# Optimization experiments

Measured on AMD Instinct MI355X. Metric: run time of the kernel, lower is better.

The kernel has to match this reference:

```python
import jax, jax.numpy as jnp
import numpy as np

N_NODES = 50000
HEADS = 4
OUT_DIM = 64
NEG_SLOPE = 0.2
BETA = 0.5
C_CONST = 1.0
EPS = 1e-16


def setup_inputs() -> dict:
    key = jax.random.key(0)
    ks = jax.random.split(key, 6)
    in_dim = 128
    x = jax.random.normal(ks[0], (N_NODES, in_dim), dtype=jnp.float32)
    edge_index = jax.random.randint(ks[1], (2, 800000), 0, N_NODES, dtype=jnp.int64)
    # GATConv params (glorot-ish scale)
    W = jax.random.normal(ks[2], (in_dim, HEADS * OUT_DIM), dtype=jnp.float32) * (1.0 / np.sqrt(in_dim))
    att_src = jax.random.normal(ks[3], (HEADS, OUT_DIM), dtype=jnp.float32) * (1.0 / np.sqrt(OUT_DIM))
    att_dst = jax.random.normal(ks[4], (HEADS, OUT_DIM), dtype=jnp.float32) * (1.0 / np.sqrt(OUT_DIM))
    bias = jnp.zeros((HEADS * OUT_DIM,), dtype=jnp.float32)
    return {"x": x, "edge_index": edge_index, "W": W, "att_src": att_src,
            "att_dst": att_dst, "bias": bias}


def _gat_conv(x, edge_index, W, att_src, att_dst, bias):
    N = x.shape[0]
    # add self loops (PyG GATConv default)
    loop = jnp.arange(N, dtype=edge_index.dtype)
    src = jnp.concatenate([edge_index[0], loop])
    dst = jnp.concatenate([edge_index[1], loop])
    # linear transform: [N, H, F]
    h = (x @ W).reshape(N, HEADS, OUT_DIM)
    # per-node attention logits: [N, H]
    a_src = jnp.einsum('nhf,hf->nh', h, att_src)
    a_dst = jnp.einsum('nhf,hf->nh', h, att_dst)
    # per-edge logits and segment softmax over destination nodes
    e = jax.nn.leaky_relu(a_src[src] + a_dst[dst], negative_slope=NEG_SLOPE)  # [E, H]
    m = jax.ops.segment_max(e, dst, num_segments=N)                           # [N, H]
    ex = jnp.exp(e - m[dst])
    s = jax.ops.segment_sum(ex, dst, num_segments=N)                          # [N, H]
    alpha = ex / (s[dst] + EPS)                                               # [E, H]
    # aggregate messages: [N, H, F]
    out = jax.ops.segment_sum(alpha[:, :, None] * h[src], dst, num_segments=N)
    return out.reshape(N, HEADS * OUT_DIM) + bias


def reference(x, edge_index, W, att_src, att_dst, bias):
    # eval mode: feature dropout and attention dropout are identity
    z = _gat_conv(x, edge_index, W, att_src, att_dst, bias)
    return BETA * z + (C_CONST - BETA) * jax.nn.elu(z)
```

## Files before the change

kernel.cpp:

```cpp
#include <hip/hip_runtime.h>
#include <hip/hip_bf16.h>

typedef unsigned short u16;
typedef __attribute__((ext_vector_type(8))) short bf16x8;
typedef __attribute__((ext_vector_type(4))) float f32x4;

#define HEADS 4
#define OUT_DIM 64
#define HF 256
#define IN_DIM 128
#define NEG_SLOPE 0.2f
#define EPSF 1e-16f

__device__ __forceinline__ float braw2f(u16 u) {
    union { float f; unsigned int i; } c; c.i = ((unsigned int)u) << 16; return c.f;
}
__device__ __forceinline__ u16 f2braw(float v) {
    __hip_bfloat16 t = __float2bfloat16(v);
    return *(u16*)&t;
}
__device__ __forceinline__ float lrelu(float e) { return e < 0.f ? NEG_SLOPE * e : e; }

__device__ __forceinline__ bool detect_i64(const int* ei) {
    return (ei[1] | ei[3] | ei[5] | ei[7] | ei[9] | ei[11] | ei[13] | ei[15]) == 0;
}
__device__ __forceinline__ void get_edge(const int* ei, int E, int t, bool i64,
                                         int& s, int& d) {
    if (t < E) {
        if (i64) { s = ei[2 * t]; d = ei[2 * (E + t)]; }
        else     { s = ei[t];     d = ei[E + t]; }
    } else {
        s = d = t - E;
    }
}

__global__ __launch_bounds__(256) void init_kernel(const float* __restrict__ W,
                                                   const float* __restrict__ att_s,
                                                   const float* __restrict__ att_d,
                                                   float* __restrict__ wa_s,
                                                   float* __restrict__ wa_d,
                                                   int* __restrict__ cnt,
                                                   int* __restrict__ cur,
                                                   int* __restrict__ gcnt,
                                                   int N, int NZ) {
    int b = blockIdx.x;
    if (b == 0 && threadIdx.x == 0) *gcnt = 0;
    if (b < NZ) {
        int i = b * 256 + threadIdx.x;
        if (i < N) { cnt[i] = 0; cur[i] = 0; }
    } else {
        for (int idx = threadIdx.x; idx < HEADS * IN_DIM; idx += 256) {
            int h = idx >> 7, k = idx & 127;
            float ss = 0.f, sd = 0.f;
            for (int f = 0; f < OUT_DIM; ++f) {
                float wv = W[k * HF + h * OUT_DIM + f];
                ss = fmaf(wv, att_s[h * OUT_DIM + f], ss);
                sd = fmaf(wv, att_d[h * OUT_DIM + f], sd);
            }
            wa_s[idx] = ss;
            wa_d[idx] = sd;
        }
    }
}

__global__ __launch_bounds__(256) void phase1_kernel(const float* __restrict__ x,
                                                     const int* __restrict__ ei,
                                                     const float* __restrict__ W,
                                                     const float* __restrict__ wa_s,
                                                     const float* __restrict__ wa_d,
                                                     float* __restrict__ a_src,
                                                     float* __restrict__ a_dst,
                                                     u16* __restrict__ xb,
                                                     u16* __restrict__ Wfrag,
                                                     int* __restrict__ cnt,
                                                     int N, int E, int NA, int NC) {
    int b = blockIdx.x;
    if (b < NA) {
        int wid = threadIdx.x >> 6;
        int l = threadIdx.x & 63;
        int g = l >> 4, c = l & 15, kc = c * 8;
        int v = b * 16 + wid * 4 + g;
        if (v >= N) return;

        const float4* xr = (const float4*)(x + (size_t)v * IN_DIM + kc);
        float4 x0 = xr[0], x1 = xr[1];

        uint4 u;
        u.x = (unsigned)f2braw(x0.x) | ((unsigned)f2braw(x0.y) << 16);
        u.y = (unsigned)f2braw(x0.z) | ((unsigned)f2braw(x0.w) << 16);
        u.z = (unsigned)f2braw(x1.x) | ((unsigned)f2braw(x1.y) << 16);
        u.w = (unsigned)f2braw(x1.z) | ((unsigned)f2braw(x1.w) << 16);
        *(uint4*)(xb + (size_t)v * IN_DIM + kc) = u;

        float ps[4], pd[4];
        #pragma unroll
        for (int h = 0; h < 4; ++h) {
            const float4* s4 = (const float4*)(wa_s + h * IN_DIM + kc);
            const float4* d4 = (const float4*)(wa_d + h * IN_DIM + kc);
            float4 s0 = s4[0], s1 = s4[1], d0 = d4[0], d1 = d4[1];
            ps[h] = x0.x*s0.x + x0.y*s0.y + x0.z*s0.z + x0.w*s0.w
                  + x1.x*s1.x + x1.y*s1.y + x1.z*s1.z + x1.w*s1.w;
            pd[h] = x0.x*d0.x + x0.y*d0.y + x0.z*d0.z + x0.w*d0.w
                  + x1.x*d1.x + x1.y*d1.y + x1.z*d1.z + x1.w*d1.w;
        }
        #pragma unroll
        for (int off = 1; off < 16; off <<= 1) {
            #pragma unroll
            for (int h = 0; h < 4; ++h) {
                ps[h] += __shfl_xor(ps[h], off);
                pd[h] += __shfl_xor(pd[h], off);
            }
        }
        if (c == 0) {
            float4 vs, vd;
            vs.x = ps[0]; vs.y = ps[1]; vs.z = ps[2]; vs.w = ps[3];
            vd.x = pd[0]; vd.y = pd[1]; vd.z = pd[2]; vd.w = pd[3];
            *(float4*)(a_src + (size_t)v * HEADS) = vs;
            *(float4*)(a_dst + (size_t)v * HEADS) = vd;
        }
    } else if (b < NA + NC) {
        int t = (b - NA) * 256 + threadIdx.x;
        if (t >= E + N) return;
        bool i64 = detect_i64(ei);
        int src, dst; get_edge(ei, E, t, i64, src, dst);
        if (src >= 0 && src < N && dst >= 0 && dst < N) atomicAdd(cnt + dst, 1);
    } else {
        int bb = b - NA - NC;
        for (int idx = bb * 256 + threadIdx.x; idx < 32768; idx += 8 * 256) {
            int j = idx & 7, l = (idx >> 3) & 63, t = (idx >> 9) & 3;
            int s = (idx >> 11) & 3, h = (idx >> 13) & 3;
            int k = s * 32 + ((l >> 4) & 3) * 8 + j;
            int col = h * OUT_DIM + t * 16 + (l & 15);
            Wfrag[idx] = f2braw(W[k * HF + col]);
        }
    }
}

__global__ __launch_bounds__(256) void offset_kernel(const int* __restrict__ cnt,
                                                     int* __restrict__ offs,
                                                     int* __restrict__ gcnt, int N) {
    int idx = blockIdx.x * 256 + threadIdx.x;
    int l = threadIdx.x & 63;
    int d = (idx < N) ? cnt[idx] : 0;
    int s = d;
    #pragma unroll
    for (int off = 1; off < 64; off <<= 1) {
        int t = __shfl_up(s, off);
        if (l >= off) s += t;
    }
    int base = 0;
    if (l == 63) base = atomicAdd(gcnt, s);
    base = __shfl(base, 63);
    if (idx < N) offs[idx] = base + s - d;
}

__global__ __launch_bounds__(256) void fill_kernel(const int* __restrict__ ei,
                                                   const int* __restrict__ offs,
                                                   int* __restrict__ cur,
                                                   int* __restrict__ slots,
                                                   uint2* __restrict__ wslots,
                                                   const float* __restrict__ a_src,
                                                   const float* __restrict__ a_dst,
                                                   int E, int N) {
    int t = blockIdx.x * 256 + threadIdx.x;
    if (t >= E + N) return;
    bool i64 = detect_i64(ei);
    int src, dst; get_edge(ei, E, t, i64, src, dst);
    if (src >= 0 && src < N && dst >= 0 && dst < N) {
        int pos = atomicAdd(cur + dst, 1);
        int idx = offs[dst] + pos;
        slots[idx] = src;
        if (wslots) {
            float4 as = ((const float4*)a_src)[src];
            float4 ad = ((const float4*)a_dst)[dst];
            float w0 = __expf(lrelu(as.x + ad.x));
            float w1 = __expf(lrelu(as.y + ad.y));
            float w2 = __expf(lrelu(as.z + ad.z));
            float w3 = __expf(lrelu(as.w + ad.w));
            uint2 wp;
            wp.x = (unsigned)f2braw(w0) | ((unsigned)f2braw(w1) << 16);
            wp.y = (unsigned)f2braw(w2) | ((unsigned)f2braw(w3) << 16);
            wslots[idx] = wp;
        }
    }
}

#define ACC_EDGE(wp, r) do { \
    float w0_ = braw2f((wp).x & 0xffff), w1_ = braw2f((wp).x >> 16); \
    float w2_ = braw2f((wp).y & 0xffff), w3_ = braw2f((wp).y >> 16); \
    ls0 += w0_; ls1 += w1_; ls2 += w2_; ls3 += w3_; \
    float xv_[8]; \
    xv_[0] = braw2f((r).x & 0xffff); xv_[1] = braw2f((r).x >> 16); \
    xv_[2] = braw2f((r).y & 0xffff); xv_[3] = braw2f((r).y >> 16); \
    xv_[4] = braw2f((r).z & 0xffff); xv_[5] = braw2f((r).z >> 16); \
    xv_[6] = braw2f((r).w & 0xffff); xv_[7] = braw2f((r).w >> 16); \
    _Pragma("unroll") \
    for (int q_ = 0; q_ < 8; ++q_) { \
        G0[q_] = fmaf(w0_, xv_[q_], G0[q_]); \
        G1[q_] = fmaf(w1_, xv_[q_], G1[q_]); \
        G2[q_] = fmaf(w2_, xv_[q_], G2[q_]); \
        G3[q_] = fmaf(w3_, xv_[q_], G3[q_]); \
    } \
} while (0)

__global__ __launch_bounds__(512) void fused_gz_kernel(const int* __restrict__ offs,
                                                       const int* __restrict__ cnt,
                                                       const int* __restrict__ slots,
                                                       const uint2* __restrict__ wslots,
                                                       const u16* __restrict__ xb,
                                                       const u16* __restrict__ Wfrag,
                                                       const float* __restrict__ bias,
                                                       float* __restrict__ out,
                                                       int N, int ET) {
    __shared__ u16 smem[32 * 520];

    int tid = threadIdx.x;
    int wid = tid >> 6;
    int l = tid & 63;
    int g = l >> 4, c = l & 15, kc = c * 8;
    int n = wid * 4 + g;
    int v = blockIdx.x * 32 + n;

    int beg = 0, end = 0;
    if (v < N) {
        beg = offs[v];
        int deg = cnt[v];
        beg = max(0, min(beg, ET));
        end = max(beg, min(beg + deg, ET));
    }

    float ls0 = 0.f, ls1 = 0.f, ls2 = 0.f, ls3 = 0.f;
    float G0[8] = {0,0,0,0,0,0,0,0};
    float G1[8] = {0,0,0,0,0,0,0,0};
    float G2[8] = {0,0,0,0,0,0,0,0};
    float G3[8] = {0,0,0,0,0,0,0,0};

    int j = beg;
    for (; j + 4 <= end; j += 4) {
        int s0 = max(0, min(slots[j],     N - 1));
        int s1 = max(0, min(slots[j + 1], N - 1));
        int s2 = max(0, min(slots[j + 2], N - 1));
        int s3 = max(0, min(slots[j + 3], N - 1));
        uint2 wp0 = wslots[j];
        uint2 wp1 = wslots[j + 1];
        uint2 wp2 = wslots[j + 2];
        uint2 wp3 = wslots[j + 3];
        uint4 r0 = *(const uint4*)(xb + (size_t)s0 * IN_DIM + kc);
        uint4 r1 = *(const uint4*)(xb + (size_t)s1 * IN_DIM + kc);
        uint4 r2 = *(const uint4*)(xb + (size_t)s2 * IN_DIM + kc);
        uint4 r3 = *(const uint4*)(xb + (size_t)s3 * IN_DIM + kc);
        ACC_EDGE(wp0, r0);
        ACC_EDGE(wp1, r1);
        ACC_EDGE(wp2, r2);
        ACC_EDGE(wp3, r3);
    }
    for (; j < end; ++j) {
        int s0 = max(0, min(slots[j], N - 1));
        uint2 wp0 = wslots[j];
        uint4 r0 = *(const uint4*)(xb + (size_t)s0 * IN_DIM + kc);
        ACC_EDGE(wp0, r0);
    }

    if (v < N) {
        float i0 = 1.f / (ls0 + EPSF), i1 = 1.f / (ls1 + EPSF);
        float i2 = 1.f / (ls2 + EPSF), i3 = 1.f / (ls3 + EPSF);
        u16* lp = smem + n * 520 + c * 8;
        #pragma unroll
        for (int h = 0; h < 4; ++h) {
            const float* G = h == 0 ? G0 : h == 1 ? G1 : h == 2 ? G2 : G3;
            float inv = h == 0 ? i0 : h == 1 ? i1 : h == 2 ? i2 : i3;
            uint4 u;
            u.x = (unsigned)f2braw(G[0] * inv) | ((unsigned)f2braw(G[1] * inv) << 16);
            u.y = (unsigned)f2braw(G[2] * inv) | ((unsigned)f2braw(G[3] * inv) << 16);
            u.z = (unsigned)f2braw(G[4] * inv) | ((unsigned)f2braw(G[5] * inv) << 16);
            u.w = (unsigned)f2braw(G[6] * inv) | ((unsigned)f2braw(G[7] * inv) << 16);
            *(uint4*)(lp + h * 128) = u;
        }
    }
    __syncthreads();

    int t = wid >> 2;
    int h = wid & 3;
    int q = l >> 4, mcol = l & 15;
    int nb = blockIdx.x * 32 + t * 16;

    const u16* lp = smem + (t * 16 + mcol) * 520 + h * 128 + q * 8;
    bf16x8 A[4];
    A[0] = *(const bf16x8*)(lp);
    A[1] = *(const bf16x8*)(lp + 32);
    A[2] = *(const bf16x8*)(lp + 64);
    A[3] = *(const bf16x8*)(lp + 96);

    f32x4 acc0 = {0.f,0.f,0.f,0.f}, acc1 = acc0, acc2 = acc0, acc3 = acc0;
    #pragma unroll
    for (int s = 0; s < 4; ++s) {
        const u16* wb = Wfrag + (((h * 4 + s) * 4) << 9) + l * 8;
        bf16x8 B0 = *(const bf16x8*)(wb);
        bf16x8 B1 = *(const bf16x8*)(wb + 512);
        bf16x8 B2 = *(const bf16x8*)(wb + 1024);
        bf16x8 B3 = *(const bf16x8*)(wb + 1536);
        acc0 = __builtin_amdgcn_mfma_f32_16x16x32_bf16(A[s], B0, acc0, 0, 0, 0);
        acc1 = __builtin_amdgcn_mfma_f32_16x16x32_bf16(A[s], B1, acc1, 0, 0, 0);
        acc2 = __builtin_amdgcn_mfma_f32_16x16x32_bf16(A[s], B2, acc2, 0, 0, 0);
        acc3 = __builtin_amdgcn_mfma_f32_16x16x32_bf16(A[s], B3, acc3, 0, 0, 0);
    }

    #pragma unroll
    for (int bt = 0; bt < 4; ++bt) {
        f32x4 a = bt == 0 ? acc0 : bt == 1 ? acc1 : bt == 2 ? acc2 : acc3;
        float b = bias[h * OUT_DIM + bt * 16 + mcol];
        #pragma unroll
        for (int r = 0; r < 4; ++r) {
            int vv = nb + q * 4 + r;
            if (vv < N) {
                float z = a[r] + b;
                float y = z > 0.f ? z : 0.5f * z + 0.5f * (__expf(z) - 1.f);
                out[(size_t)vv * HF + h * OUT_DIM + bt * 16 + mcol] = y;
            }
        }
    }
}

__global__ __launch_bounds__(512) void gather_bf_kernel(const int* __restrict__ offs,
                                                        const int* __restrict__ cnt,
                                                        const int* __restrict__ slots,
                                                        const u16* __restrict__ xb,
                                                        const float* __restrict__ a_src,
                                                        const float* __restrict__ a_dst,
                                                        u16* __restrict__ Gout, int N, int ET) {
    int v = (blockIdx.x * 512 + threadIdx.x) >> 6;
    int l = threadIdx.x & 63;
    if (v >= N) return;
    int h = l >> 4, c = l & 15, kc = c * 8;

    int beg = offs[v];
    int deg = cnt[v];
    beg = max(0, min(beg, ET));
    int end = max(beg, min(beg + deg, ET));
    float adh = a_dst[v * HEADS + h];

    float ls = 0.f;
    float G[8] = {0.f,0.f,0.f,0.f,0.f,0.f,0.f,0.f};

    int j = beg;
    for (; j + 4 <= end; j += 4) {
        int s0 = max(0, min(slots[j],     N - 1));
        int s1 = max(0, min(slots[j + 1], N - 1));
        int s2 = max(0, min(slots[j + 2], N - 1));
        int s3 = max(0, min(slots[j + 3], N - 1));
        float w0 = __expf(lrelu(a_src[s0 * HEADS + h] + adh));
        float w1 = __expf(lrelu(a_src[s1 * HEADS + h] + adh));
        float w2 = __expf(lrelu(a_src[s2 * HEADS + h] + adh));
        float w3 = __expf(lrelu(a_src[s3 * HEADS + h] + adh));
        uint4 r0 = *(const uint4*)(xb + (size_t)s0 * IN_DIM + kc);
        uint4 r1 = *(const uint4*)(xb + (size_t)s1 * IN_DIM + kc);
        uint4 r2 = *(const uint4*)(xb + (size_t)s2 * IN_DIM + kc);
        uint4 r3 = *(const uint4*)(xb + (size_t)s3 * IN_DIM + kc);
        ls += (w0 + w1) + (w2 + w3);
        unsigned ua[4];
        ua[0]=r0.x; ua[1]=r0.y; ua[2]=r0.z; ua[3]=r0.w;
        #pragma unroll
        for (int q = 0; q < 4; ++q) {
            G[2*q]   = fmaf(w0, braw2f(ua[q] & 0xffff), G[2*q]);
            G[2*q+1] = fmaf(w0, braw2f(ua[q] >> 16),    G[2*q+1]);
        }
        ua[0]=r1.x; ua[1]=r1.y; ua[2]=r1.z; ua[3]=r1.w;
        #pragma unroll
        for (int q = 0; q < 4; ++q) {
            G[2*q]   = fmaf(w1, braw2f(ua[q] & 0xffff), G[2*q]);
            G[2*q+1] = fmaf(w1, braw2f(ua[q] >> 16),    G[2*q+1]);
        }
        ua[0]=r2.x; ua[1]=r2.y; ua[2]=r2.z; ua[3]=r2.w;
        #pragma unroll
        for (int q = 0; q < 4; ++q) {
            G[2*q]   = fmaf(w2, braw2f(ua[q] & 0xffff), G[2*q]);
            G[2*q+1] = fmaf(w2, braw2f(ua[q] >> 16),    G[2*q+1]);
        }
        ua[0]=r3.x; ua[1]=r3.y; ua[2]=r3.z; ua[3]=r3.w;
        #pragma unroll
        for (int q = 0; q < 4; ++q) {
            G[2*q]   = fmaf(w3, braw2f(ua[q] & 0xffff), G[2*q]);
            G[2*q+1] = fmaf(w3, braw2f(ua[q] >> 16),    G[2*q+1]);
        }
    }
    for (; j < end; ++j) {
        int s0 = max(0, min(slots[j], N - 1));
        float w0 = __expf(lrelu(a_src[s0 * HEADS + h] + adh));
        uint4 r0 = *(const uint4*)(xb + (size_t)s0 * IN_DIM + kc);
        ls += w0;
        unsigned ua[4]; ua[0]=r0.x; ua[1]=r0.y; ua[2]=r0.z; ua[3]=r0.w;
        #pragma unroll
        for (int q = 0; q < 4; ++q) {
            G[2*q]   = fmaf(w0, braw2f(ua[q] & 0xffff), G[2*q]);
            G[2*q+1] = fmaf(w0, braw2f(ua[q] >> 16),    G[2*q+1]);
        }
    }

    float inv = 1.f / (ls + EPSF);
    uint4 u;
    u.x = (unsigned)f2braw(G[0] * inv) | ((unsigned)f2braw(G[1] * inv) << 16);
    u.y = (unsigned)f2braw(G[2] * inv) | ((unsigned)f2braw(G[3] * inv) << 16);
    u.z = (unsigned)f2braw(G[4] * inv) | ((unsigned)f2braw(G[5] * inv) << 16);
    u.w = (unsigned)f2braw(G[6] * inv) | ((unsigned)f2braw(G[7] * inv) << 16);
    *(uint4*)(Gout + (size_t)v * 512 + h * 128 + kc) = u;
}

__global__ __launch_bounds__(512) void gather_f32_kernel(const int* __restrict__ offs,
                                                         const int* __restrict__ cnt,
                                                         const int* __restrict__ slots,
                                                         const float* __restrict__ x,
                                                         const float* __restrict__ a_src,
                                                         const float* __restrict__ a_dst,
                                                         u16* __restrict__ Gout, int N, int ET) {
    int v = (blockIdx.x * 512 + threadIdx.x) >> 6;
    int l = threadIdx.x & 63;
    if (v >= N) return;
    int h = l >> 4, c = l & 15, kc = c * 8;

    int beg = offs[v];
    int deg = cnt[v];
    beg = max(0, min(beg, ET));
    int end = max(beg, min(beg + deg, ET));
    float adh = a_dst[v * HEADS + h];

    float ls = 0.f;
    float G[8] = {0.f,0.f,0.f,0.f,0.f,0.f,0.f,0.f};
    for (int j = beg; j < end; ++j) {
        int s0 = max(0, min(slots[j], N - 1));
        float w0 = __expf(lrelu(a_src[s0 * HEADS + h] + adh));
        const float4* xr0 = (const float4*)(x + (size_t)s0 * IN_DIM + kc);
        float4 a0 = xr0[0], b0 = xr0[1];
        ls += w0;
        G[0]=fmaf(w0,a0.x,G[0]); G[1]=fmaf(w0,a0.y,G[1]);
        G[2]=fmaf(w0,a0.z,G[2]); G[3]=fmaf(w0,a0.w,G[3]);
        G[4]=fmaf(w0,b0.x,G[4]); G[5]=fmaf(w0,b0.y,G[5]);
        G[6]=fmaf(w0,b0.z,G[6]); G[7]=fmaf(w0,b0.w,G[7]);
    }
    float inv = 1.f / (ls + EPSF);
    uint4 u;
    u.x = (unsigned)f2braw(G[0] * inv) | ((unsigned)f2braw(G[1] * inv) << 16);
    u.y = (unsigned)f2braw(G[2] * inv) | ((unsigned)f2braw(G[3] * inv) << 16);
    u.z = (unsigned)f2braw(G[4] * inv) | ((unsigned)f2braw(G[5] * inv) << 16);
    u.w = (unsigned)f2braw(G[6] * inv) | ((unsigned)f2braw(G[7] * inv) << 16);
    *(uint4*)(Gout + (size_t)v * 512 + h * 128 + kc) = u;
}

__global__ __launch_bounds__(256) void zgemm_kernel(const u16* __restrict__ Wfrag,
                                                    const float* __restrict__ bias,
                                                    float* __restrict__ out, int N) {
    int h = threadIdx.x >> 6;
    int l = threadIdx.x & 63;
    int q = l >> 4, mcol = l & 15;
    int nb = blockIdx.x * 16;

    const u16* G = (const u16*)out;
    bool valid = (nb + mcol) < N;
    int vA = valid ? nb + mcol : N - 1;
    const u16* gp = G + (size_t)vA * 512 + h * 128 + q * 8;
    bf16x8 A[4];
    A[0] = *(const bf16x8*)(gp);
    A[1] = *(const bf16x8*)(gp + 32);
    A[2] = *(const bf16x8*)(gp + 64);
    A[3] = *(const bf16x8*)(gp + 96);
    if (!valid) {
        bf16x8 zz = {0,0,0,0,0,0,0,0};
        A[0] = zz; A[1] = zz; A[2] = zz; A[3] = zz;
    }

    f32x4 acc0 = {0.f,0.f,0.f,0.f}, acc1 = acc0, acc2 = acc0, acc3 = acc0;
    #pragma unroll
    for (int s = 0; s < 4; ++s) {
        const u16* wb = Wfrag + (((h * 4 + s) * 4) << 9) + l * 8;
        bf16x8 B0 = *(const bf16x8*)(wb);
        bf16x8 B1 = *(const bf16x8*)(wb + 512);
        bf16x8 B2 = *(const bf16x8*)(wb + 1024);
        bf16x8 B3 = *(const bf16x8*)(wb + 1536);
        acc0 = __builtin_amdgcn_mfma_f32_16x16x32_bf16(A[s], B0, acc0, 0, 0, 0);
        acc1 = __builtin_amdgcn_mfma_f32_16x16x32_bf16(A[s], B1, acc1, 0, 0, 0);
        acc2 = __builtin_amdgcn_mfma_f32_16x16x32_bf16(A[s], B2, acc2, 0, 0, 0);
        acc3 = __builtin_amdgcn_mfma_f32_16x16x32_bf16(A[s], B3, acc3, 0, 0, 0);
    }

    #pragma unroll
    for (int t = 0; t < 4; ++t) {
        f32x4 a = t == 0 ? acc0 : t == 1 ? acc1 : t == 2 ? acc2 : acc3;
        float b = bias[h * OUT_DIM + t * 16 + mcol];
        #pragma unroll
        for (int r = 0; r < 4; ++r) {
            int v = nb + q * 4 + r;
            if (v < N) {
                float z = a[r] + b;
                float y = z > 0.f ? z : 0.5f * z + 0.5f * (__expf(z) - 1.f);
                out[(size_t)v * HF + h * OUT_DIM + t * 16 + mcol] = y;
            }
        }
    }
}

extern "C" void kernel_launch(void* const* d_in, const int* in_sizes, int n_in,
                              void* d_out, int out_size, void* d_ws, size_t ws_size,
                              hipStream_t stream) {
    const float* x       = (const float*)d_in[0];
    const int*   ei      = (const int*)d_in[1];
    const float* W       = (const float*)d_in[2];
    const float* att_src = (const float*)d_in[3];
    const float* att_dst = (const float*)d_in[4];
    const float* bias    = (const float*)d_in[5];

    const int N = in_sizes[0] / IN_DIM;
    const int E = in_sizes[1] / 2;
    const int ET = E + N;
    const int NT = (N + 255) / 256;

    char* ws = (char*)d_ws;
    size_t off = 0;
    float* wa_s   = (float*)(ws + off); off += HEADS * IN_DIM * 4;
    float* wa_d   = (float*)(ws + off); off += HEADS * IN_DIM * 4;
    u16*   Wfrag  = (u16*)(ws + off);   off += 32768 * 2;
    float* a_src  = (float*)(ws + off); off += (size_t)N * HEADS * 4;
    float* a_dst  = (float*)(ws + off); off += (size_t)N * HEADS * 4;
    int*   offs   = (int*)(ws + off);   off += ((size_t)N * 4 + 15) & ~(size_t)15;
    int*   cnt    = (int*)(ws + off);   off += ((size_t)N * 4 + 15) & ~(size_t)15;
    int*   cur    = (int*)(ws + off);   off += ((size_t)N * 4 + 15) & ~(size_t)15;
    int*   gcnt   = (int*)(ws + off);   off += 64;
    int*   slots  = (int*)(ws + off);   off += ((size_t)ET * 4 + 15) & ~(size_t)15;
    u16*   xb     = (u16*)(ws + off);   size_t need_bf = off + (size_t)N * IN_DIM * 2;
    uint2* wslots = (uint2*)(ws + need_bf);
    size_t need_w = need_bf + (size_t)ET * 8;
    bool use_bf = (ws_size >= need_bf);
    bool use_w  = (ws_size >= need_w);

    const int NA = (N + 15) / 16;
    const int NC = (ET + 255) / 256;

    init_kernel<<<NT + 1, 256, 0, stream>>>(W, att_src, att_dst, wa_s, wa_d,
                                            cnt, cur, gcnt, N, NT);
    phase1_kernel<<<NA + NC + 8, 256, 0, stream>>>(x, ei, W, wa_s, wa_d, a_src, a_dst,
                                                   use_bf ? xb : (u16*)d_out,
                                                   Wfrag, cnt, N, E, NA, NC);
    offset_kernel<<<NT, 256, 0, stream>>>(cnt, offs, gcnt, N);
    fill_kernel<<<(ET + 255) / 256, 256, 0, stream>>>(ei, offs, cur, slots,
                                                      use_w ? wslots : (uint2*)0,
                                                      a_src, a_dst, E, N);
    if (use_w) {
        fused_gz_kernel<<<(N + 31) / 32, 512, 0, stream>>>(offs, cnt, slots, wslots,
                                                           xb, Wfrag, bias,
                                                           (float*)d_out, N, ET);
    } else if (use_bf) {
        gather_bf_kernel<<<(N * 64 + 511) / 512, 512, 0, stream>>>(offs, cnt, slots, xb,
                                                                   a_src, a_dst,
                                                                   (u16*)d_out, N, ET);
        zgemm_kernel<<<(N + 15) / 16, 256, 0, stream>>>(Wfrag, bias, (float*)d_out, N);
    } else {
        gather_f32_kernel<<<(N * 64 + 511) / 512, 512, 0, stream>>>(offs, cnt, slots, x,
                                                                    a_src, a_dst,
                                                                    (u16*)d_out, N, ET);
        zgemm_kernel<<<(N + 15) / 16, 256, 0, stream>>>(Wfrag, bias, (float*)d_out, N);
    }
}
```

Measured before the change: 260.6 us.

## Sort nodes by degree via histogram bucketing before fused gather-GEMM

Adds a degree histogram in the offset pass, a single-block bucket scan, and a scatter kernel that builds a degree-sorted node permutation. The fused gather/GEMM kernel then processes nodes in that order and writes outputs via the permuted indices. The aim is to balance per-wavefront and per-block work, since the 16-lane groups in a block otherwise wait on the highest-degree node. It costs two extra kernel launches and makes the output stores scattered instead of contiguous.

```diff
diff --git a/kernel.cpp b/kernel.cpp
--- a/kernel.cpp
+++ b/kernel.cpp
@@ -42,9 +42,15 @@
                                                    int* __restrict__ cnt,
                                                    int* __restrict__ cur,
                                                    int* __restrict__ gcnt,
+                                                   int* __restrict__ hist,
+                                                   int* __restrict__ bcur,
                                                    int N, int NZ) {
     int b = blockIdx.x;
-    if (b == 0 && threadIdx.x == 0) *gcnt = 0;
+    if (b == 0) {
+        if (threadIdx.x == 0) *gcnt = 0;
+        hist[threadIdx.x] = 0;
+        bcur[threadIdx.x] = 0;
+    }
     if (b < NZ) {
         int i = b * 256 + threadIdx.x;
         if (i < N) { cnt[i] = 0; cur[i] = 0; }
@@ -138,10 +144,17 @@
 
 __global__ __launch_bounds__(256) void offset_kernel(const int* __restrict__ cnt,
                                                      int* __restrict__ offs,
-                                                     int* __restrict__ gcnt, int N) {
+                                                     int* __restrict__ gcnt,
+                                                     int* __restrict__ hist, int N) {
+    __shared__ int lh[256];
+    lh[threadIdx.x] = 0;
+    __syncthreads();
+
     int idx = blockIdx.x * 256 + threadIdx.x;
     int l = threadIdx.x & 63;
     int d = (idx < N) ? cnt[idx] : 0;
+    if (idx < N) atomicAdd(lh + min(max(d, 0), 255), 1);
+
     int s = d;
     #pragma unroll
     for (int off = 1; off < 64; off <<= 1) {
@@ -152,6 +165,38 @@
     if (l == 63) base = atomicAdd(gcnt, s);
     base = __shfl(base, 63);
     if (idx < N) offs[idx] = base + s - d;
+
+    __syncthreads();
+    if (lh[threadIdx.x]) atomicAdd(hist + threadIdx.x, lh[threadIdx.x]);
+}
+
+__global__ __launch_bounds__(256) void bscan_kernel(const int* __restrict__ hist,
+                                                    int* __restrict__ bbase, int N) {
+    __shared__ int sc[256];
+    int tid = threadIdx.x;
+    sc[tid] = hist[tid];
+    __syncthreads();
+    #pragma unroll
+    for (int off = 1; off < 256; off <<= 1) {
+        int t = (tid >= off) ? sc[tid - off] : 0;
+        __syncthreads();
+        sc[tid] += t;
+        __syncthreads();
+    }
+    bbase[tid] = N - sc[tid];
+}
+
+__global__ __launch_bounds__(256) void scatter_kernel(const int* __restrict__ cnt,
+                                                      const int* __restrict__ bbase,
+                                                      int* __restrict__ bcur,
+                                                      int* __restrict__ perm, int N) {
+    int idx = blockIdx.x * 256 + threadIdx.x;
+    if (idx < N) {
+        int b = min(max(cnt[idx], 0), 255);
+        int pos = atomicAdd(bcur + b, 1);
+        int p = bbase[b] + pos;
+        if (p >= 0 && p < N) perm[p] = idx;
+    }
 }
 
 __global__ __launch_bounds__(256) void fill_kernel(const int* __restrict__ ei,
@@ -203,7 +248,8 @@
     } \
 } while (0)
 
-__global__ __launch_bounds__(512) void fused_gz_kernel(const int* __restrict__ offs,
+__global__ __launch_bounds__(512) void fused_gz_kernel(const int* __restrict__ perm,
+                                                       const int* __restrict__ offs,
                                                        const int* __restrict__ cnt,
                                                        const int* __restrict__ slots,
                                                        const uint2* __restrict__ wslots,
@@ -213,16 +259,24 @@
                                                        float* __restrict__ out,
                                                        int N, int ET) {
     __shared__ u16 smem[32 * 520];
+    __shared__ int pvals[32];
 
     int tid = threadIdx.x;
     int wid = tid >> 6;
     int l = tid & 63;
     int g = l >> 4, c = l & 15, kc = c * 8;
     int n = wid * 4 + g;
-    int v = blockIdx.x * 32 + n;
+    int pidx = blockIdx.x * 32 + n;
+
+    int v = -1;
+    if (pidx < N) {
+        v = perm[pidx];
+        if (v < 0 || v >= N) v = -1;
+    }
+    if (c == 0) pvals[n] = v;
 
     int beg = 0, end = 0;
-    if (v < N) {
+    if (v >= 0) {
         beg = offs[v];
         int deg = cnt[v];
         beg = max(0, min(beg, ET));
@@ -261,7 +315,7 @@
         ACC_EDGE(wp0, r0);
     }
 
-    if (v < N) {
+    if (v >= 0) {
         float i0 = 1.f / (ls0 + EPSF), i1 = 1.f / (ls1 + EPSF);
         float i2 = 1.f / (ls2 + EPSF), i3 = 1.f / (ls3 + EPSF);
         u16* lp = smem + n * 520 + c * 8;
@@ -282,7 +336,6 @@
     int t = wid >> 2;
     int h = wid & 3;
     int q = l >> 4, mcol = l & 15;
-    int nb = blockIdx.x * 32 + t * 16;
 
     const u16* lp = smem + (t * 16 + mcol) * 520 + h * 128 + q * 8;
     bf16x8 A[4];
@@ -311,8 +364,8 @@
         float b = bias[h * OUT_DIM + bt * 16 + mcol];
         #pragma unroll
         for (int r = 0; r < 4; ++r) {
-            int vv = nb + q * 4 + r;
-            if (vv < N) {
+            int vv = pvals[t * 16 + q * 4 + r];
+            if (vv >= 0) {
                 float z = a[r] + b;
                 float y = z > 0.f ? z : 0.5f * z + 0.5f * (__expf(z) - 1.f);
                 out[(size_t)vv * HF + h * OUT_DIM + bt * 16 + mcol] = y;
@@ -523,6 +576,10 @@
     int*   cnt    = (int*)(ws + off);   off += ((size_t)N * 4 + 15) & ~(size_t)15;
     int*   cur    = (int*)(ws + off);   off += ((size_t)N * 4 + 15) & ~(size_t)15;
     int*   gcnt   = (int*)(ws + off);   off += 64;
+    int*   hist   = (int*)(ws + off);   off += 256 * 4;
+    int*   bbase  = (int*)(ws + off);   off += 256 * 4;
+    int*   bcur   = (int*)(ws + off);   off += 256 * 4;
+    int*   perm   = (int*)(ws + off);   off += ((size_t)N * 4 + 15) & ~(size_t)15;
     int*   slots  = (int*)(ws + off);   off += ((size_t)ET * 4 + 15) & ~(size_t)15;
     u16*   xb     = (u16*)(ws + off);   size_t need_bf = off + (size_t)N * IN_DIM * 2;
     uint2* wslots = (uint2*)(ws + need_bf);
@@ -534,17 +591,19 @@
     const int NC = (ET + 255) / 256;
 
     init_kernel<<<NT + 1, 256, 0, stream>>>(W, att_src, att_dst, wa_s, wa_d,
-                                            cnt, cur, gcnt, N, NT);
+                                            cnt, cur, gcnt, hist, bcur, N, NT);
     phase1_kernel<<<NA + NC + 8, 256, 0, stream>>>(x, ei, W, wa_s, wa_d, a_src, a_dst,
                                                    use_bf ? xb : (u16*)d_out,
                                                    Wfrag, cnt, N, E, NA, NC);
-    offset_kernel<<<NT, 256, 0, stream>>>(cnt, offs, gcnt, N);
+    offset_kernel<<<NT, 256, 0, stream>>>(cnt, offs, gcnt, hist, N);
     fill_kernel<<<(ET + 255) / 256, 256, 0, stream>>>(ei, offs, cur, slots,
                                                       use_w ? wslots : (uint2*)0,
                                                       a_src, a_dst, E, N);
     if (use_w) {
-        fused_gz_kernel<<<(N + 31) / 32, 512, 0, stream>>>(offs, cnt, slots, wslots,
-                                                           xb, Wfrag, bias,
+        bscan_kernel<<<1, 256, 0, stream>>>(hist, bbase, N);
+        scatter_kernel<<<NT, 256, 0, stream>>>(cnt, bbase, bcur, perm, N);
+        fused_gz_kernel<<<(N + 31) / 32, 512, 0, stream>>>(perm, offs, cnt, slots,
+                                                           wslots, xb, Wfrag, bias,
                                                            (float*)d_out, N, ET);
     } else if (use_bf) {
         gather_bf_kernel<<<(N * 64 + 511) / 512, 512, 0, stream>>>(offs, cnt, slots, xb,
```

After: 390.0 us. +49.6%, slower.
